# Kernel tuning notes

Measured on AMD Instinct MI355X. Metric: run time of the kernel, lower is better.

The kernel has to match this reference:

```python
import jax, jax.numpy as jnp
import numpy as np
import itertools

# Per-group attribute cardinalities (product = number of prototypes per group)
GROUP_DIMS = {
    "gender": [2],
    "hair": [5, 3],
    "top": [8, 5],
    "pants": [8, 5],
    "shoes": [6, 4],
}
TAU = 0.07  # softmax temperature for prototype similarity
B, D = 32768, 512


def _affinity(dims):
    # Faithful to _build_group_affinity: A[i,j] = fraction of matching sub-attribute values
    combos = np.array(list(itertools.product(*[range(d) for d in dims])), dtype=np.int32)  # [K, n_attrs]
    mat = (combos[:, None, :] == combos[None, :, :]).mean(-1).astype(np.float32)  # [K, K]
    return jnp.asarray(mat)


def _l2(v):
    return v / (jnp.linalg.norm(v, axis=-1, keepdims=True) + 1e-6)


def setup_inputs() -> dict:
    key = jax.random.key(0)
    ks = jax.random.split(key, 1 + len(GROUP_DIMS))
    inp = {"x": jax.random.normal(ks[0], (B, D), dtype=jnp.float32)}
    for k, (name, dims) in zip(ks[1:], GROUP_DIMS.items()):
        K = int(np.prod(dims))
        # matches nn.Parameter(torch.randn(K, D) * 0.01)
        inp[f"P_{name}"] = jax.random.normal(k, (K, D), dtype=jnp.float32) * 0.01
    return inp


def reference(x, P_gender, P_hair, P_top, P_pants, P_shoes):
    protos = {"gender": P_gender, "hair": P_hair, "top": P_top, "pants": P_pants, "shoes": P_shoes}
    xn = _l2(x)  # [B, D]
    outs = []
    for name, P in protos.items():
        A = _affinity(GROUP_DIMS[name])          # [K, K] constant affinity buffer
        logits = (xn @ _l2(P).T) / TAU           # [B, K] cosine-similarity prototype lookup
        q = jax.nn.softmax(logits, axis=-1)      # soft assignment
        q_aff = q @ A                            # affinity-weighted assignment
        q_aff = q_aff / (q_aff.sum(-1, keepdims=True) + 1e-6)
        outs.append(q_aff @ P)                   # [B, D] affinity-smoothed quantized feature
    return jnp.stack(outs, axis=1)               # [B, n_groups, D]
```

## Files before the change

### kernel.cpp

```cpp
#include <hip/hip_runtime.h>
#include <hip/hip_bf16.h>
#include <math.h>


constexpr int D    = 512;
constexpr int KTOT = 121;
constexpr float TAU = 0.07f;

constexpr int GB[5]  = {0, 2, 17, 57, 97};
constexpr int GK[5]  = {2, 15, 40, 40, 24};
constexpr int GD2[5] = {1, 3, 5, 5, 4};
constexpr int GNA[5] = {1, 2, 2, 2, 2};
constexpr int KS0[5] = {0, 0, 0, 1, 3};
constexpr int KS1[5] = {1, 1, 2, 4, 4};

using f32x4 = __attribute__((ext_vector_type(4))) float;
using s16x8 = __attribute__((ext_vector_type(8))) short;

__device__ __forceinline__ const float* pick(int k,
    const float* P0, const float* P1, const float* P2, const float* P3, const float* P4,
    int* kl) {
  if (k < 2)  { *kl = k;      return P0; }
  if (k < 17) { *kl = k - 2;  return P1; }
  if (k < 57) { *kl = k - 17; return P2; }
  if (k < 97) { *kl = k - 57; return P3; }
  *kl = k - 97; return P4;
}

__device__ __forceinline__ short f2bf(float f) {
  __hip_bfloat16 h = __float2bfloat16(f);
  return *reinterpret_cast<short*>(&h);
}

__global__ void prep_norms(const float* __restrict__ P0, const float* __restrict__ P1,
                           const float* __restrict__ P2, const float* __restrict__ P3,
                           const float* __restrict__ P4, float* __restrict__ invn) {
  int k = blockIdx.x;
  int kl; const float* P = pick(k, P0, P1, P2, P3, P4, &kl);
  const float* row = P + (size_t)kl * D;
  float s = 0.f;
  for (int d = threadIdx.x; d < D; d += 64) { float v = row[d]; s += v * v; }
  #pragma unroll
  for (int m = 1; m < 64; m <<= 1) s += __shfl_xor(s, m);
  if (threadIdx.x == 0) invn[k] = 1.f / (sqrtf(s) + 1e-6f);
}

__global__ void prep_pnbf(const float* __restrict__ P0, const float* __restrict__ P1,
                          const float* __restrict__ P2, const float* __restrict__ P3,
                          const float* __restrict__ P4, const float* __restrict__ invn,
                          unsigned short* __restrict__ pnbf) {
  int idx = blockIdx.x * 256 + threadIdx.x;
  int blk = idx >> 9, e = idx & 511;
  int lane = e >> 3, j = e & 7;
  int ct = blk >> 4, s = blk & 15;
  int col = ct * 16 + (lane & 15);
  int k   = s * 32 + (lane >> 4) * 8 + j;
  float v = 0.f;
  if (col < KTOT) {
    int kl; const float* P = pick(col, P0, P1, P2, P3, P4, &kl);
    v = P[(size_t)kl * D + k] * invn[col];
  }
  pnbf[idx] = (unsigned short)f2bf(v);
}

__global__ void prep_mptbf(const float* __restrict__ P0, const float* __restrict__ P1,
                           const float* __restrict__ P2, const float* __restrict__ P3,
                           const float* __restrict__ P4, unsigned short* __restrict__ mptbf) {
  int idx = blockIdx.x * 256 + threadIdx.x;
  int blk = idx >> 9, e = idx & 511;
  int lane = e >> 3, j = e & 7;
  int c = blk >> 2, ks = blk & 3;
  int gd = c * 16 + (lane & 15);
  int k  = ks * 32 + (lane >> 4) * 8 + j;
  int g = gd >> 9, d = gd & (D - 1);
  float v = 0.f;
  if (k >= GB[g] && k < GB[g] + GK[g]) {
    int kl = k - GB[g];
    const float* P = (g == 0) ? P0 : (g == 1) ? P1 : (g == 2) ? P2 : (g == 3) ? P3 : P4;
    int d2 = GD2[g], na = GNA[g], K = GK[g];
    int a1 = kl / d2, a2 = kl % d2;
    float s = 0.f, m = 0.f;
    for (int jj = 0; jj < K; jj++) {
      float aff;
      if (na == 1) {
        aff = (jj == kl) ? 1.f : 0.f;
      } else {
        int b1 = jj / d2, b2 = jj % d2;
        aff = 0.5f * (float)((a1 == b1) + (a2 == b2));
      }
      s += aff;
      m += aff * P[(size_t)jj * D + d];
    }
    v = m / (s + 1e-6f);
  }
  mptbf[idx] = (unsigned short)f2bf(v);
}

template <int G>
__device__ __forceinline__ void phase2_group(
    const s16x8 (&af2)[4], const unsigned short* __restrict__ mptbf,
    float* __restrict__ ob, float* __restrict__ obase, int ch, int lane) {
  const int l15 = lane & 15, hi = lane >> 4;
  #pragma unroll 1
  for (int i = 0; i < 4; ++i) {
    const int s = G * 8 + i * 2 + ch;
    const unsigned short* bp = mptbf + (size_t)(s * 4) * 4 * 512 + lane * 8;
    f32x4 a0 = (f32x4){0.f, 0.f, 0.f, 0.f}, a1 = a0, a2 = a0, a3 = a0;
    #pragma unroll
    for (int ks = KS0[G]; ks < KS1[G]; ++ks) {
      s16x8 b0 = *(const s16x8*)(bp + (0 * 4 + ks) * 512);
      s16x8 b1 = *(const s16x8*)(bp + (1 * 4 + ks) * 512);
      s16x8 b2 = *(const s16x8*)(bp + (2 * 4 + ks) * 512);
      s16x8 b3 = *(const s16x8*)(bp + (3 * 4 + ks) * 512);
      a0 = __builtin_amdgcn_mfma_f32_16x16x32_bf16(b0, af2[ks], a0, 0, 0, 0);
      a1 = __builtin_amdgcn_mfma_f32_16x16x32_bf16(b1, af2[ks], a1, 0, 0, 0);
      a2 = __builtin_amdgcn_mfma_f32_16x16x32_bf16(b2, af2[ks], a2, 0, 0, 0);
      a3 = __builtin_amdgcn_mfma_f32_16x16x32_bf16(b3, af2[ks], a3, 0, 0, 0);
    }
    *(f32x4*)&ob[l15 * 68 +  0 + hi * 4] = a0;
    *(f32x4*)&ob[l15 * 68 + 16 + hi * 4] = a1;
    *(f32x4*)&ob[l15 * 68 + 32 + hi * 4] = a2;
    *(f32x4*)&ob[l15 * 68 + 48 + hi * 4] = a3;
    float* gp = obase + (size_t)s * 64 + l15 * 4;
    #pragma unroll
    for (int i2 = 0; i2 < 4; ++i2) {
      const int row = i2 * 4 + hi;
      f32x4 v = *(const f32x4*)&ob[row * 68 + l15 * 4];
      __builtin_nontemporal_store(v, (f32x4*)(gp + (size_t)row * (5 * D)));
    }
  }
}

__global__ __launch_bounds__(512, 4) void fused_main(
    const float* __restrict__ x, const unsigned short* __restrict__ pnbf,
    const unsigned short* __restrict__ mptbf, float* __restrict__ out) {
  __shared__ __align__(16) float smem[8704];
  __shared__ float xsqs[64];
  float (*lred)[65] = (float (*)[65])smem;

  const int tid  = threadIdx.x;
  const int lane = tid & 63;
  const int w    = __builtin_amdgcn_readfirstlane(tid >> 6);
  const int r0   = blockIdx.x * 64;

  const int wr = (w & 3) << 4;
  const int ch = w >> 2;
  const int ko = (lane >> 4) << 3;

  {
    const int arow = wr + (lane & 15);
    const float* xrow = x + (size_t)(r0 + arow) * D + ko;

    f32x4 acc[4];
    #pragma unroll
    for (int t = 0; t < 4; ++t) acc[t] = (f32x4){0.f, 0.f, 0.f, 0.f};
    float xsq = 0.f;

    #pragma unroll 4
    for (int s = 0; s < 16; ++s) {
      float4 a0 = *(const float4*)(xrow + s * 32);
      float4 a1 = *(const float4*)(xrow + s * 32 + 4);
      xsq += a0.x * a0.x + a0.y * a0.y + a0.z * a0.z + a0.w * a0.w
           + a1.x * a1.x + a1.y * a1.y + a1.z * a1.z + a1.w * a1.w;
      s16x8 af;
      af[0] = f2bf(a0.x); af[1] = f2bf(a0.y); af[2] = f2bf(a0.z); af[3] = f2bf(a0.w);
      af[4] = f2bf(a1.x); af[5] = f2bf(a1.y); af[6] = f2bf(a1.z); af[7] = f2bf(a1.w);
      #pragma unroll
      for (int t = 0; t < 4; ++t) {
        s16x8 bfv = *(const s16x8*)(pnbf + (size_t)(((ch << 2) + t) * 16 + s) * 512 + lane * 8);
        acc[t] = __builtin_amdgcn_mfma_f32_16x16x32_bf16(af, bfv, acc[t], 0, 0, 0);
      }
    }

    xsq += __shfl_xor(xsq, 16);
    xsq += __shfl_xor(xsq, 32);
    if (w < 4 && lane < 16) xsqs[wr + lane] = xsq;

    const int drow = wr + ((lane >> 4) << 2);
    #pragma unroll
    for (int t = 0; t < 4; ++t) {
      const int col = (ch << 6) + (t << 4) + (lane & 15);
      #pragma unroll
      for (int j = 0; j < 4; ++j) lred[col][drow + j] = acc[t][j];
    }
  }
  __syncthreads();

  if (w < 5) {
    const int g = w;
    const float scale = 1.f / ((sqrtf(xsqs[lane]) + 1e-6f) * TAU);
    float mx = -1e30f;
    for (int kk = 0; kk < GK[g]; ++kk)
      mx = fmaxf(mx, lred[GB[g] + kk][lane]);
    float E = 0.f;
    for (int kk = 0; kk < GK[g]; ++kk) {
      float e = __expf((lred[GB[g] + kk][lane] - mx) * scale);
      lred[GB[g] + kk][lane] = e;
      E += e;
    }
    const float inv = 1.f / E;
    for (int kk = 0; kk < GK[g]; ++kk) lred[GB[g] + kk][lane] *= inv;
  }
  __syncthreads();

  s16x8 af2[4];
  {
    const int ar = wr + (lane & 15);
    #pragma unroll
    for (int s = 0; s < 4; ++s) {
      const int kbase = s * 32 + ko;
      s16x8 f;
      #pragma unroll
      for (int j = 0; j < 8; ++j) f[j] = f2bf(lred[kbase + j][ar]);
      af2[s] = f;
    }
  }
  __syncthreads();

  {
    float* ob    = smem + w * (16 * 68);
    float* obase = out + (size_t)(r0 + wr) * (5 * D);

    phase2_group<0>(af2, mptbf, ob, obase, ch, lane);
    phase2_group<1>(af2, mptbf, ob, obase, ch, lane);
    phase2_group<2>(af2, mptbf, ob, obase, ch, lane);
    phase2_group<3>(af2, mptbf, ob, obase, ch, lane);
    phase2_group<4>(af2, mptbf, ob, obase, ch, lane);
  }
}

extern "C" void kernel_launch(void* const* d_in, const int* in_sizes, int n_in,
                              void* d_out, int out_size, void* d_ws, size_t ws_size,
                              hipStream_t stream) {
  const float* x  = (const float*)d_in[0];
  const float* P0 = (const float*)d_in[1];
  const float* P1 = (const float*)d_in[2];
  const float* P2 = (const float*)d_in[3];
  const float* P3 = (const float*)d_in[4];
  const float* P4 = (const float*)d_in[5];
  float* out = (float*)d_out;

  unsigned short* pnbf  = (unsigned short*)d_ws;
  unsigned short* mptbf = pnbf + 128 * 512;
  float* invn = (float*)(mptbf + 640 * 512);

  prep_norms<<<dim3(121), dim3(64), 0, stream>>>(P0, P1, P2, P3, P4, invn);
  prep_pnbf<<<dim3(256), dim3(256), 0, stream>>>(P0, P1, P2, P3, P4, invn, pnbf);
  prep_mptbf<<<dim3(1280), dim3(256), 0, stream>>>(P0, P1, P2, P3, P4, mptbf);
  fused_main<<<dim3(512), dim3(512), 0, stream>>>(x, pnbf, mptbf, out);
}
```

Baseline: 117.7 us.

## Merge prep kernels into one launch and halve rows per main-kernel block

Replaces the three preprocessing kernels (prototype norms, normalized bf16 prototype tiles, affinity-smoothed prototype tiles) with one kernel. The first 8 blocks compute norms in shared memory and write the normalized tiles, and the remaining blocks build the smoothed matrix. This removes two launches and the invn round-trip through global memory. The main fused kernel now handles 32 rows per 256-thread block with twice as many blocks, shrinking LDS use and rebalancing the softmax so wave 0 handles groups 0 and 4. In exchange, prototype tiles are reloaded by more blocks.

```diff
diff --git a/kernel.cpp b/kernel.cpp
--- a/kernel.cpp
+++ b/kernel.cpp
@@ -32,68 +32,84 @@
   return *reinterpret_cast<short*>(&h);
 }
 
-__global__ void prep_norms(const float* __restrict__ P0, const float* __restrict__ P1,
-                           const float* __restrict__ P2, const float* __restrict__ P3,
-                           const float* __restrict__ P4, float* __restrict__ invn) {
-  int k = blockIdx.x;
-  int kl; const float* P = pick(k, P0, P1, P2, P3, P4, &kl);
-  const float* row = P + (size_t)kl * D;
-  float s = 0.f;
-  for (int d = threadIdx.x; d < D; d += 64) { float v = row[d]; s += v * v; }
-  #pragma unroll
-  for (int m = 1; m < 64; m <<= 1) s += __shfl_xor(s, m);
-  if (threadIdx.x == 0) invn[k] = 1.f / (sqrtf(s) + 1e-6f);
-}
-
-__global__ void prep_pnbf(const float* __restrict__ P0, const float* __restrict__ P1,
-                          const float* __restrict__ P2, const float* __restrict__ P3,
-                          const float* __restrict__ P4, const float* __restrict__ invn,
-                          unsigned short* __restrict__ pnbf) {
-  int idx = blockIdx.x * 256 + threadIdx.x;
-  int blk = idx >> 9, e = idx & 511;
-  int lane = e >> 3, j = e & 7;
-  int ct = blk >> 4, s = blk & 15;
-  int col = ct * 16 + (lane & 15);
-  int k   = s * 32 + (lane >> 4) * 8 + j;
-  float v = 0.f;
-  if (col < KTOT) {
-    int kl; const float* P = pick(col, P0, P1, P2, P3, P4, &kl);
-    v = P[(size_t)kl * D + k] * invn[col];
-  }
-  pnbf[idx] = (unsigned short)f2bf(v);
-}
-
-__global__ void prep_mptbf(const float* __restrict__ P0, const float* __restrict__ P1,
-                           const float* __restrict__ P2, const float* __restrict__ P3,
-                           const float* __restrict__ P4, unsigned short* __restrict__ mptbf) {
-  int idx = blockIdx.x * 256 + threadIdx.x;
-  int blk = idx >> 9, e = idx & 511;
-  int lane = e >> 3, j = e & 7;
-  int c = blk >> 2, ks = blk & 3;
-  int gd = c * 16 + (lane & 15);
-  int k  = ks * 32 + (lane >> 4) * 8 + j;
-  int g = gd >> 9, d = gd & (D - 1);
-  float v = 0.f;
-  if (k >= GB[g] && k < GB[g] + GK[g]) {
-    int kl = k - GB[g];
-    const float* P = (g == 0) ? P0 : (g == 1) ? P1 : (g == 2) ? P2 : (g == 3) ? P3 : P4;
-    int d2 = GD2[g], na = GNA[g], K = GK[g];
-    int a1 = kl / d2, a2 = kl % d2;
-    float s = 0.f, m = 0.f;
-    for (int jj = 0; jj < K; jj++) {
-      float aff;
-      if (na == 1) {
-        aff = (jj == kl) ? 1.f : 0.f;
-      } else {
-        int b1 = jj / d2, b2 = jj % d2;
-        aff = 0.5f * (float)((a1 == b1) + (a2 == b2));
-      }
-      s += aff;
-      m += aff * P[(size_t)jj * D + d];
-    }
-    v = m / (s + 1e-6f);
-  }
-  mptbf[idx] = (unsigned short)f2bf(v);
+__global__ __launch_bounds__(256) void prep_all(
+    const float* __restrict__ P0, const float* __restrict__ P1,
+    const float* __restrict__ P2, const float* __restrict__ P3,
+    const float* __restrict__ P4, unsigned short* __restrict__ pnbf,
+    unsigned short* __restrict__ mptbf) {
+  const int tid = threadIdx.x;
+  if (blockIdx.x < 8) {
+    const int ct = blockIdx.x;
+    __shared__ float lsum[16][17];
+    __shared__ float linv[16];
+    {
+      const int i = tid >> 4, part = tid & 15;
+      const int col = ct * 16 + i;
+      float s = 0.f;
+      if (col < KTOT) {
+        int kl; const float* P = pick(col, P0, P1, P2, P3, P4, &kl);
+        const float* row = P + (size_t)kl * D + part * 32;
+        #pragma unroll
+        for (int e = 0; e < 32; ++e) { float v = row[e]; s += v * v; }
+      }
+      lsum[i][part] = s;
+    }
+    __syncthreads();
+    if (tid < 16) {
+      float s = 0.f;
+      #pragma unroll
+      for (int p = 0; p < 16; ++p) s += lsum[tid][p];
+      linv[tid] = 1.f / (sqrtf(s) + 1e-6f);
+    }
+    __syncthreads();
+    for (int s = 0; s < 16; ++s) {
+      #pragma unroll
+      for (int half = 0; half < 2; ++half) {
+        const int e = tid + half * 256;
+        const int lane = e >> 3, j = e & 7;
+        const int col = ct * 16 + (lane & 15);
+        const int k   = s * 32 + (lane >> 4) * 8 + j;
+        float v = 0.f;
+        if (col < KTOT) {
+          int kl; const float* P = pick(col, P0, P1, P2, P3, P4, &kl);
+          v = P[(size_t)kl * D + k] * linv[lane & 15];
+        }
+        pnbf[(size_t)(ct * 16 + s) * 512 + e] = (unsigned short)f2bf(v);
+      }
+    }
+  } else {
+    const int c2 = blockIdx.x - 8;
+    const int c = c2 >> 2, ks = c2 & 3;
+    #pragma unroll
+    for (int half = 0; half < 2; ++half) {
+      const int e = tid + half * 256;
+      const int lane = e >> 3, j = e & 7;
+      const int gd = c * 16 + (lane & 15);
+      const int k  = ks * 32 + (lane >> 4) * 8 + j;
+      const int g = gd >> 9, d = gd & (D - 1);
+      float v = 0.f;
+      if (k >= GB[g] && k < GB[g] + GK[g]) {
+        int kl = k - GB[g];
+        const float* P = (g == 0) ? P0 : (g == 1) ? P1 : (g == 2) ? P2 : (g == 3) ? P3 : P4;
+        int d2 = GD2[g], na = GNA[g], K = GK[g];
+        int a1 = kl / d2, a2 = kl % d2;
+        float s = 0.f, m = 0.f;
+        for (int jj = 0; jj < K; jj++) {
+          float aff;
+          if (na == 1) {
+            aff = (jj == kl) ? 1.f : 0.f;
+          } else {
+            int b1 = jj / d2, b2 = jj % d2;
+            aff = 0.5f * (float)((a1 == b1) + (a2 == b2));
+          }
+          s += aff;
+          m += aff * P[(size_t)jj * D + d];
+        }
+        v = m / (s + 1e-6f);
+      }
+      mptbf[(size_t)c2 * 512 + e] = (unsigned short)f2bf(v);
+    }
+  }
 }
 
 template <int G>
@@ -131,20 +147,20 @@
   }
 }
 
-__global__ __launch_bounds__(512, 4) void fused_main(
+__global__ __launch_bounds__(256, 4) void fused_main(
     const float* __restrict__ x, const unsigned short* __restrict__ pnbf,
     const unsigned short* __restrict__ mptbf, float* __restrict__ out) {
-  __shared__ __align__(16) float smem[8704];
-  __shared__ float xsqs[64];
-  float (*lred)[65] = (float (*)[65])smem;
+  __shared__ __align__(16) float smem[4352];
+  __shared__ float xsqs[32];
+  float (*lred)[33] = (float (*)[33])smem;
 
   const int tid  = threadIdx.x;
   const int lane = tid & 63;
   const int w    = __builtin_amdgcn_readfirstlane(tid >> 6);
-  const int r0   = blockIdx.x * 64;
-
-  const int wr = (w & 3) << 4;
-  const int ch = w >> 2;
+  const int r0   = blockIdx.x * 32;
+
+  const int wr = (w & 1) << 4;
+  const int ch = w >> 1;
   const int ko = (lane >> 4) << 3;
 
   {
@@ -174,7 +190,7 @@
 
     xsq += __shfl_xor(xsq, 16);
     xsq += __shfl_xor(xsq, 32);
-    if (w < 4 && lane < 16) xsqs[wr + lane] = xsq;
+    if (ch == 0 && lane < 16) xsqs[wr + lane] = xsq;
 
     const int drow = wr + ((lane >> 4) << 2);
     #pragma unroll
@@ -186,20 +202,23 @@
   }
   __syncthreads();
 
-  if (w < 5) {
-    const int g = w;
+  if (lane < 32) {
     const float scale = 1.f / ((sqrtf(xsqs[lane]) + 1e-6f) * TAU);
-    float mx = -1e30f;
-    for (int kk = 0; kk < GK[g]; ++kk)
-      mx = fmaxf(mx, lred[GB[g] + kk][lane]);
-    float E = 0.f;
-    for (int kk = 0; kk < GK[g]; ++kk) {
-      float e = __expf((lred[GB[g] + kk][lane] - mx) * scale);
-      lred[GB[g] + kk][lane] = e;
-      E += e;
-    }
-    const float inv = 1.f / E;
-    for (int kk = 0; kk < GK[g]; ++kk) lred[GB[g] + kk][lane] *= inv;
+    const int gfirst = (w == 0) ? 0 : w;
+    const int glast  = (w == 0) ? 4 : w;
+    for (int g = gfirst; g <= glast; g += (w == 0) ? 4 : 1) {
+      float mx = -1e30f;
+      for (int kk = 0; kk < GK[g]; ++kk)
+        mx = fmaxf(mx, lred[GB[g] + kk][lane]);
+      float E = 0.f;
+      for (int kk = 0; kk < GK[g]; ++kk) {
+        float e = __expf((lred[GB[g] + kk][lane] - mx) * scale);
+        lred[GB[g] + kk][lane] = e;
+        E += e;
+      }
+      const float inv = 1.f / E;
+      for (int kk = 0; kk < GK[g]; ++kk) lred[GB[g] + kk][lane] *= inv;
+    }
   }
   __syncthreads();
 
@@ -242,10 +261,7 @@
 
   unsigned short* pnbf  = (unsigned short*)d_ws;
   unsigned short* mptbf = pnbf + 128 * 512;
-  float* invn = (float*)(mptbf + 640 * 512);
-
-  prep_norms<<<dim3(121), dim3(64), 0, stream>>>(P0, P1, P2, P3, P4, invn);
-  prep_pnbf<<<dim3(256), dim3(256), 0, stream>>>(P0, P1, P2, P3, P4, invn, pnbf);
-  prep_mptbf<<<dim3(1280), dim3(256), 0, stream>>>(P0, P1, P2, P3, P4, mptbf);
-  fused_main<<<dim3(512), dim3(512), 0, stream>>>(x, pnbf, mptbf, out);
-}
+
+  prep_all<<<dim3(648), dim3(256), 0, stream>>>(P0, P1, P2, P3, P4, pnbf, mptbf);
+  fused_main<<<dim3(1024), dim3(256), 0, stream>>>(x, pnbf, mptbf, out);
+}
```

New measurement: 116.0 us. About the same (-1.4%).
